# Optimization experiments

Hardware: AMD Instinct MI355X
Metric: run time of the kernel (lower is better)

The kernel has to match this reference:

```python
import jax, jax.numpy as jnp
import numpy as np

B = 4096
FEAT = 512
EMB = 64
HID = 1024
NUM_CLASSES = 64   # == option_num == noise_lib_Y.shape[0]
LIB_X = 256
LIB_Y = 256
OUT_J = 256


def setup_inputs() -> dict:
    key = jax.random.key(0)
    ks = jax.random.split(key, 16)
    s = lambda k, shape, fan: jax.random.normal(k, shape, jnp.float32) / np.sqrt(fan)
    d_in = FEAT + EMB
    return {
        "state": jax.random.normal(ks[0], (B, FEAT), jnp.float32),
        "option": jax.random.randint(ks[1], (B,), 0, NUM_CLASSES, jnp.int64),
        "embed_table": s(ks[2], (NUM_CLASSES, EMB), EMB),
        "Wx1": s(ks[3], (d_in, HID), d_in), "bx1": jnp.zeros((HID,), jnp.float32),
        "Wx2": s(ks[4], (HID, LIB_X), HID), "bx2": jnp.zeros((LIB_X,), jnp.float32),
        "Wy1": s(ks[5], (d_in, HID), d_in), "by1": jnp.zeros((HID,), jnp.float32),
        "Wy2": s(ks[6], (HID, LIB_Y), HID), "by2": jnp.zeros((LIB_Y,), jnp.float32),
        "noise_lib_X": s(ks[7], (LIB_X, OUT_J), LIB_X),
        "noise_lib_Y": s(ks[8], (NUM_CLASSES, LIB_Y, OUT_J), LIB_Y),
    }


def _mlp(x, W1, b1, W2, b2):
    # MLP_RELU, layer_num=2: Linear -> ReLU -> Linear
    h = jax.nn.relu(x @ W1 + b1)
    return h @ W2 + b2


def reference(state, option, embed_table, Wx1, bx1, Wx2, bx2,
              Wy1, by1, Wy2, by2, noise_lib_X, noise_lib_Y):
    option_embed = embed_table[option]                      # [B, EMB]
    all_state = jnp.concatenate([state, option_embed], axis=-1)
    cls_X = _mlp(all_state, Wx1, bx1, Wx2, bx2)             # [B, LIB_X]
    cls_Y = _mlp(all_state, Wy1, by1, Wy2, by2)             # [B, LIB_Y]
    # Original: einsum('bi,mij->bmj') then mask with one_hot(option).
    # Mathematically identical gather-then-matmul (honors the routing sparsity):
    noise_Y_sel = noise_lib_Y[option]                       # [B, LIB_Y, OUT_J]
    generate_noise_Y = jnp.einsum('bi,bij->bj', cls_Y, noise_Y_sel)
    generate_noise_X = cls_X @ noise_lib_X                  # [B, OUT_J]
    return (generate_noise_X, generate_noise_Y)
```

## Files before the change

kernel.cpp:

```cpp
#include <hip/hip_runtime.h>

typedef unsigned short u16;
typedef unsigned int u32;

using f32x4  = __attribute__((ext_vector_type(4))) float;
using bf16x8 = __attribute__((ext_vector_type(8))) __bf16;

#define DEV __device__ __forceinline__

DEV u16 f2bf(float f) {
  union { float f; u32 u; } x; x.f = f;
  return (u16)((x.u + 0x7fffu + ((x.u >> 16) & 1u)) >> 16);
}
DEV float bf2f(u16 h) {
  union { u32 u; float f; } x; x.u = ((u32)h) << 16;
  return x.f;
}

DEV void async_cp16(const u16* g, u16* l) {
  __builtin_amdgcn_global_load_lds((const __attribute__((address_space(1))) void*)g,
                                   (__attribute__((address_space(3))) void*)l,
                                   16, 0, 0);
}

static constexpr int BATCH = 4096;
static constexpr int FEAT  = 512;
static constexpr int EMB   = 64;
static constexpr int HID   = 1024;
static constexpr int NC    = 64;
static constexpr int DIN   = 576;
static constexpr int LIB   = 256;

DEV void detect_lite(const u32* __restrict__ sraw, const u32* __restrict__ oraw,
                     int* isf32, int* ostr) {
  __shared__ int cib, conz;
  const int t = threadIdx.x;
  if (t == 0) { cib = 0; conz = 0; }
  u32 w = sraw[t];
  u32 e = (w >> 7) & 0xFFu;
  unsigned long long m1 = __ballot(e >= 100 && e <= 142);
  unsigned long long m2 = __ballot((t & 1) && oraw[t] != 0);
  __syncthreads();
  if ((t & 63) == 0) {
    atomicAdd(&cib, __popcll(m1));
    atomicAdd(&conz, __popcll(m2));
  }
  __syncthreads();
  *isf32 = (cib < 128) ? 1 : 0;
  *ostr  = (conz == 0) ? 2 : 1;
}

DEV void do_transpose64(const void* __restrict__ in, size_t in_off,
                        u16* __restrict__ out, int R, int C,
                        int by, int bx, int isf32) {
  __shared__ u16 tile[64 * 72];
  const int t = threadIdx.x;
  {
    const int r = t >> 2, c0 = (t & 3) * 16;
    size_t off = in_off + (size_t)(by * 64 + r) * C + (bx * 64 + c0);
    u16 v[16];
    if (isf32) {
      const float4* s = (const float4*)((const float*)in + off);
      float4 a0 = s[0], a1 = s[1], a2 = s[2], a3 = s[3];
      v[0] = f2bf(a0.x); v[1] = f2bf(a0.y); v[2]  = f2bf(a0.z); v[3]  = f2bf(a0.w);
      v[4] = f2bf(a1.x); v[5] = f2bf(a1.y); v[6]  = f2bf(a1.z); v[7]  = f2bf(a1.w);
      v[8] = f2bf(a2.x); v[9] = f2bf(a2.y); v[10] = f2bf(a2.z); v[11] = f2bf(a2.w);
      v[12] = f2bf(a3.x); v[13] = f2bf(a3.y); v[14] = f2bf(a3.z); v[15] = f2bf(a3.w);
    } else {
      const uint4* s = (const uint4*)((const u16*)in + off);
      *(uint4*)&v[0] = s[0];
      *(uint4*)&v[8] = s[1];
    }
    *(uint4*)&tile[r * 72 + c0]     = *(uint4*)&v[0];
    *(uint4*)&tile[r * 72 + c0 + 8] = *(uint4*)&v[8];
  }
  __syncthreads();
  {
    const int c = t & 63, rs = (t >> 6) * 16;
    u16 w[16];
#pragma unroll
    for (int i = 0; i < 16; ++i) w[i] = tile[(rs + i) * 72 + c];
    size_t oo = (size_t)(bx * 64 + c) * R + (by * 64 + rs);
    *(uint4*)&out[oo]     = *(uint4*)&w[0];
    *(uint4*)&out[oo + 8] = *(uint4*)&w[8];
  }
}

struct PrepArgs {
  const void *state, *emb, *Wx1, *Wy1, *Wx2, *Wy2, *nX;
  const int* opt;
  u16 *all_state, *WT1x, *WT1y, *WT2x, *WT2y, *XT;
};
static constexpr int PB_CONCAT = BATCH * 36 / 256;
static constexpr int PB_WT1 = (DIN / 64) * (HID / 64);
static constexpr int PB_WT2 = (HID / 64) * (LIB / 64);
static constexpr int PB_XT  = (LIB / 64) * (LIB / 64);
static constexpr int PREP_BLOCKS = PB_CONCAT + 2 * PB_WT1 + 2 * PB_WT2 + PB_XT;

__global__ __launch_bounds__(256) void prep_k(PrepArgs a) {
  int isf32, os;
  detect_lite((const u32*)a.state, (const u32*)a.opt, &isf32, &os);
  int bid = blockIdx.x;
  if (bid < PB_CONCAT) {
    int idx = bid * 256 + threadIdx.x;
    int b = idx / 36, ch = idx % 36;
    const void* base;
    size_t srcoff;
    if (ch < 32) { base = a.state; srcoff = (size_t)b * FEAT + ch * 16; }
    else {
      base = a.emb;
      srcoff = (size_t)a.opt[(size_t)b * os] * EMB + (ch - 32) * 16;
    }
    u16 o[16];
    if (isf32) {
      const float4* s = (const float4*)((const float*)base + srcoff);
      float4 a0 = s[0], a1 = s[1], a2 = s[2], a3 = s[3];
      o[0] = f2bf(a0.x); o[1] = f2bf(a0.y); o[2]  = f2bf(a0.z); o[3]  = f2bf(a0.w);
      o[4] = f2bf(a1.x); o[5] = f2bf(a1.y); o[6]  = f2bf(a1.z); o[7]  = f2bf(a1.w);
      o[8] = f2bf(a2.x); o[9] = f2bf(a2.y); o[10] = f2bf(a2.z); o[11] = f2bf(a2.w);
      o[12] = f2bf(a3.x); o[13] = f2bf(a3.y); o[14] = f2bf(a3.z); o[15] = f2bf(a3.w);
    } else {
      const uint4* s = (const uint4*)((const u16*)base + srcoff);
      *(uint4*)&o[0] = s[0];
      *(uint4*)&o[8] = s[1];
    }
    u16* dst = a.all_state + (size_t)b * DIN + ch * 16;
    *(uint4*)dst       = *(const uint4*)&o[0];
    *(uint4*)(dst + 8) = *(const uint4*)&o[8];
    return;
  }
  bid -= PB_CONCAT;
  if (bid < PB_WT1) { do_transpose64(a.Wx1, 0, a.WT1x, DIN, HID, bid >> 4, bid & 15, isf32); return; }
  bid -= PB_WT1;
  if (bid < PB_WT1) { do_transpose64(a.Wy1, 0, a.WT1y, DIN, HID, bid >> 4, bid & 15, isf32); return; }
  bid -= PB_WT1;
  if (bid < PB_WT2) { do_transpose64(a.Wx2, 0, a.WT2x, HID, LIB, bid >> 2, bid & 3, isf32); return; }
  bid -= PB_WT2;
  if (bid < PB_WT2) { do_transpose64(a.Wy2, 0, a.WT2y, HID, LIB, bid >> 2, bid & 3, isf32); return; }
  bid -= PB_WT2;
  do_transpose64(a.nX, 0, a.XT, LIB, LIB, bid >> 2, bid & 3, isf32);
}

template <int BM, int BN, bool RELU>
DEV void gemm_tile(u16* lds, const u16* __restrict__ A, const u16* __restrict__ Bt,
                   const void* bias, void* C, int N, int K, int m0, int n0,
                   int isf32, bool cf32) {
  constexpr int WM = BM / 2, WN = BN / 2, TM = WM / 16, TN = WN / 16;
  u16* As = lds;
  u16* Bs = lds + BM * 64;
  const int t = threadIdx.x;
  const int lane = t & 63, wid = t >> 6;
  const int wm = wid >> 1, wn = wid & 1;
  const int lr = lane & 15, lq = lane >> 4;
  f32x4 acc[TM][TN] = {};
  for (int k0 = 0; k0 < K; k0 += 64) {
    __syncthreads();
#pragma unroll
    for (int sl = 0; sl < 2; ++sl) {
#pragma unroll
      for (int u = 0; u < BM / 64; ++u) {
        int unit = u * 256 + t;
        int r = unit >> 2, c8 = (unit & 3) * 8;
        async_cp16(A + (size_t)(m0 + r) * K + (k0 + sl * 32 + c8),
                   &As[(sl * BM + r) * 32 + c8]);
      }
#pragma unroll
      for (int u = 0; u < BN / 64; ++u) {
        int unit = u * 256 + t;
        int r = unit >> 2, c8 = (unit & 3) * 8;
        async_cp16(Bt + (size_t)(n0 + r) * K + (k0 + sl * 32 + c8),
                   &Bs[(sl * BN + r) * 32 + c8]);
      }
    }
    __syncthreads();
#pragma unroll
    for (int sl = 0; sl < 2; ++sl) {
      bf16x8 av[TM], bv[TN];
#pragma unroll
      for (int i = 0; i < TM; ++i)
        av[i] = *(const bf16x8*)&As[(sl * BM + wm * WM + i * 16 + lr) * 32 + lq * 8];
#pragma unroll
      for (int j = 0; j < TN; ++j)
        bv[j] = *(const bf16x8*)&Bs[(sl * BN + wn * WN + j * 16 + lr) * 32 + lq * 8];
#pragma unroll
      for (int i = 0; i < TM; ++i)
#pragma unroll
        for (int j = 0; j < TN; ++j)
          acc[i][j] = __builtin_amdgcn_mfma_f32_16x16x32_bf16(av[i], bv[j], acc[i][j], 0, 0, 0);
    }
  }
#pragma unroll
  for (int j = 0; j < TN; ++j) {
    const int gc = n0 + wn * WN + j * 16 + lr;
    const float bval = bias
        ? (isf32 ? ((const float*)bias)[gc] : bf2f(((const u16*)bias)[gc]))
        : 0.f;
#pragma unroll
    for (int i = 0; i < TM; ++i) {
      const int gr = m0 + wm * WM + i * 16 + lq * 4;
#pragma unroll
      for (int r = 0; r < 4; ++r) {
        float v = acc[i][j][r] + bval;
        if (RELU) v = fmaxf(v, 0.f);
        const size_t idx = (size_t)(gr + r) * N + gc;
        if (cf32) ((float*)C)[idx] = v;
        else      ((u16*)C)[idx] = f2bf(v);
      }
    }
  }
}

struct GArg { const u16* A; const u16* Bt; const void* bias; void* C; int cflag; };

template <int BM, int BN, bool RELU>
__global__ __launch_bounds__(256) void gemm_bt(GArg g0, GArg g1, int N, int K,
                                               const void* state, const void* opt) {
  __shared__ __align__(16) u16 lds[(BM + BN) * 64];
  int isf32, os;
  detect_lite((const u32*)state, (const u32*)opt, &isf32, &os);
  const GArg g = blockIdx.z ? g1 : g0;
  gemm_tile<BM, BN, RELU>(lds, g.A, g.Bt, g.bias, g.C, N, K,
                          blockIdx.y * BM, blockIdx.x * BN,
                          isf32, g.cflag && isf32);
}

struct TailArgs {
  const u16 *cls_x, *XT, *cls_y;
  const void *nY, *state;
  const int* opt;
  void* out;
};

__global__ __launch_bounds__(256) void tail_k(TailArgs a) {
  __shared__ __align__(16) u16 lds[25216];
  __shared__ int wcnt[4], lbase;
  int isf32, os;
  detect_lite((const u32*)a.state, (const u32*)a.opt, &isf32, &os);
  const bool of32 = (isf32 != 0);
  const int t = threadIdx.x;
  const int lane = t & 63, w = t >> 6, lr = lane & 15, lq = lane >> 4;

  if (blockIdx.x < 256) {
    const int m0 = (blockIdx.x >> 2) * 64, n0 = (blockIdx.x & 3) * 64;
    gemm_tile<64, 64, false>(lds, a.cls_x, a.XT, nullptr, a.out,
                             LIB, LIB, m0, n0, isf32, of32);
    return;
  }

  u16* Bts  = lds;
  u16* Asm  = lds + 16896;
  u16* list = lds + 21120;
  const int rb = blockIdx.x - 256;
  const int m = rb >> 2, n0 = (rb & 3) * 64;

#pragma unroll
  for (int pass = 0; pass < 4; ++pass) {
    const int k = pass * 64 + (t >> 2), nc = (t & 3) * 16;
    const size_t off = ((size_t)m * LIB + k) * LIB + n0 + nc;
    u16 v[16];
    if (isf32) {
      const float4* s = (const float4*)((const float*)a.nY + off);
      float4 a0 = s[0], a1 = s[1], a2 = s[2], a3 = s[3];
      v[0] = f2bf(a0.x); v[1] = f2bf(a0.y); v[2]  = f2bf(a0.z); v[3]  = f2bf(a0.w);
      v[4] = f2bf(a1.x); v[5] = f2bf(a1.y); v[6]  = f2bf(a1.z); v[7]  = f2bf(a1.w);
      v[8] = f2bf(a2.x); v[9] = f2bf(a2.y); v[10] = f2bf(a2.z); v[11] = f2bf(a2.w);
      v[12] = f2bf(a3.x); v[13] = f2bf(a3.y); v[14] = f2bf(a3.z); v[15] = f2bf(a3.w);
    } else {
      const uint4* s = (const uint4*)((const u16*)a.nY + off);
      *(uint4*)&v[0] = s[0];
      *(uint4*)&v[8] = s[1];
    }
#pragma unroll
    for (int j = 0; j < 16; ++j) Bts[(nc + j) * 264 + k] = v[j];
  }

  if (t == 0) lbase = 0;
  __syncthreads();
  for (int base = 0; base < BATCH; base += 256) {
    const int b = base + t;
    const int e = a.opt[(size_t)b * os];
    unsigned long long mk = __ballot(e == m);
    if (lane == 0) wcnt[w] = __popcll(mk);
    __syncthreads();
    int wpre = lbase;
    for (int i = 0; i < w; ++i) wpre += wcnt[i];
    const int mypre = __popcll(mk & ((1ull << lane) - 1ull));
    if (e == m) list[wpre + mypre] = (u16)b;
    __syncthreads();
    if (t == 0) lbase += wcnt[0] + wcnt[1] + wcnt[2] + wcnt[3];
  }
  __syncthreads();
  const int cnt = lbase;
  const size_t out_off = (size_t)BATCH * LIB;

  for (int ch = 0; ch < cnt; ch += 16) {
    __syncthreads();
    {
      const int r = t >> 4, cb = (t & 15) * 16;
      if (ch + r < cnt) {
        const u16* src = a.cls_y + (size_t)list[ch + r] * LIB + cb;
        *(uint4*)&Asm[r * 264 + cb]     = *(const uint4*)src;
        *(uint4*)&Asm[r * 264 + cb + 8] = *(const uint4*)(src + 8);
      } else {
        uint4 z{0, 0, 0, 0};
        *(uint4*)&Asm[r * 264 + cb]     = z;
        *(uint4*)&Asm[r * 264 + cb + 8] = z;
      }
    }
    __syncthreads();
    f32x4 acc = {};
#pragma unroll
    for (int kk = 0; kk < LIB; kk += 32) {
      bf16x8 av = *(const bf16x8*)&Asm[lr * 264 + kk + lq * 8];
      bf16x8 bv = *(const bf16x8*)&Bts[(w * 16 + lr) * 264 + kk + lq * 8];
      acc = __builtin_amdgcn_mfma_f32_16x16x32_bf16(av, bv, acc, 0, 0, 0);
    }
#pragma unroll
    for (int r = 0; r < 4; ++r) {
      const int rowc = lq * 4 + r;
      if (ch + rowc < cnt) {
        const size_t oi = out_off + (size_t)list[ch + rowc] * LIB
                        + (n0 + w * 16 + lr);
        if (of32) ((float*)a.out)[oi] = acc[r];
        else      ((u16*)a.out)[oi] = f2bf(acc[r]);
      }
    }
  }
}

extern "C" void kernel_launch(void* const* d_in, const int* in_sizes, int n_in,
                              void* d_out, int out_size, void* d_ws, size_t ws_size,
                              hipStream_t stream) {
  char* p = (char*)d_ws;
  auto alloc = [&](size_t bytes) { char* r = p; p += (bytes + 255) & ~(size_t)255; return r; };
  u16* all_state = (u16*)alloc((size_t)BATCH * DIN * 2);
  u16* h_x   = (u16*)alloc((size_t)BATCH * HID * 2);
  u16* h_y   = (u16*)alloc((size_t)BATCH * HID * 2);
  u16* cls_x = (u16*)alloc((size_t)BATCH * LIB * 2);
  u16* cls_y = (u16*)alloc((size_t)BATCH * LIB * 2);
  u16* WT1x  = (u16*)alloc((size_t)HID * DIN * 2);
  u16* WT1y  = (u16*)alloc((size_t)HID * DIN * 2);
  u16* WT2x  = (u16*)alloc((size_t)LIB * HID * 2);
  u16* WT2y  = (u16*)alloc((size_t)LIB * HID * 2);
  u16* XT    = (u16*)alloc((size_t)LIB * LIB * 2);

  const void* state = d_in[0];
  const void* opt   = d_in[1];

  PrepArgs pa;
  pa.state = state; pa.opt = (const int*)opt; pa.emb = d_in[2];
  pa.Wx1 = d_in[3]; pa.Wx2 = d_in[5]; pa.Wy1 = d_in[7]; pa.Wy2 = d_in[9];
  pa.nX = d_in[11];
  pa.all_state = all_state; pa.WT1x = WT1x; pa.WT1y = WT1y;
  pa.WT2x = WT2x; pa.WT2y = WT2y; pa.XT = XT;
  prep_k<<<PREP_BLOCKS, 256, 0, stream>>>(pa);

  GArg g1x{all_state, WT1x, d_in[4], h_x, 0}, g1y{all_state, WT1y, d_in[8], h_y, 0};
  gemm_bt<128, 128, true><<<dim3(HID / 128, BATCH / 128, 2), 256, 0, stream>>>(
      g1x, g1y, HID, DIN, state, opt);

  GArg g2x{h_x, WT2x, d_in[6], cls_x, 0}, g2y{h_y, WT2y, d_in[10], cls_y, 0};
  gemm_bt<64, 64, false><<<dim3(LIB / 64, BATCH / 64, 2), 256, 0, stream>>>(
      g2x, g2y, LIB, HID, state, opt);

  TailArgs ta{cls_x, XT, cls_y, d_in[12], state, (const int*)opt, d_out};
  tail_k<<<512, 256, 0, stream>>>(ta);
}
```

Baseline: 156.6 us.

## Fold noise_lib_X into second X-layer weights to skip the cls_X GEMM

The product Wx2 @ noise_lib_X and the bias bx2 @ noise_lib_X are precomputed in the prep kernel, so the second X-branch GEMM writes generate_noise_X directly and the tail kernel no longer runs the cls_X @ XT GEMM. This removes one B×256×256 GEMM and the cls_x round trip through memory, in exchange for a small weight-only GEMM and a serial bias dot product in prep, plus an extra bf16 rounding of the fused weight. The GEMM grid axes are also swapped so that blockIdx.x walks the batch rows.

```diff
diff --git a/kernel.cpp b/kernel.cpp
--- a/kernel.cpp
+++ b/kernel.cpp
@@ -50,27 +50,30 @@
   *ostr  = (conz == 0) ? 2 : 1;
 }
 
-DEV void do_transpose64(const void* __restrict__ in, size_t in_off,
+DEV void load16_bf(u16* v, const void* __restrict__ in, size_t off, int isf32) {
+  if (isf32) {
+    const float4* s = (const float4*)((const float*)in + off);
+    float4 a0 = s[0], a1 = s[1], a2 = s[2], a3 = s[3];
+    v[0] = f2bf(a0.x); v[1] = f2bf(a0.y); v[2]  = f2bf(a0.z); v[3]  = f2bf(a0.w);
+    v[4] = f2bf(a1.x); v[5] = f2bf(a1.y); v[6]  = f2bf(a1.z); v[7]  = f2bf(a1.w);
+    v[8] = f2bf(a2.x); v[9] = f2bf(a2.y); v[10] = f2bf(a2.z); v[11] = f2bf(a2.w);
+    v[12] = f2bf(a3.x); v[13] = f2bf(a3.y); v[14] = f2bf(a3.z); v[15] = f2bf(a3.w);
+  } else {
+    const uint4* s = (const uint4*)((const u16*)in + off);
+    *(uint4*)&v[0] = s[0];
+    *(uint4*)&v[8] = s[1];
+  }
+}
+
+DEV void do_transpose64(u16* lds, const void* __restrict__ in,
                         u16* __restrict__ out, int R, int C,
                         int by, int bx, int isf32) {
-  __shared__ u16 tile[64 * 72];
+  u16* tile = lds;
   const int t = threadIdx.x;
   {
     const int r = t >> 2, c0 = (t & 3) * 16;
-    size_t off = in_off + (size_t)(by * 64 + r) * C + (bx * 64 + c0);
     u16 v[16];
-    if (isf32) {
-      const float4* s = (const float4*)((const float*)in + off);
-      float4 a0 = s[0], a1 = s[1], a2 = s[2], a3 = s[3];
-      v[0] = f2bf(a0.x); v[1] = f2bf(a0.y); v[2]  = f2bf(a0.z); v[3]  = f2bf(a0.w);
-      v[4] = f2bf(a1.x); v[5] = f2bf(a1.y); v[6]  = f2bf(a1.z); v[7]  = f2bf(a1.w);
-      v[8] = f2bf(a2.x); v[9] = f2bf(a2.y); v[10] = f2bf(a2.z); v[11] = f2bf(a2.w);
-      v[12] = f2bf(a3.x); v[13] = f2bf(a3.y); v[14] = f2bf(a3.z); v[15] = f2bf(a3.w);
-    } else {
-      const uint4* s = (const uint4*)((const u16*)in + off);
-      *(uint4*)&v[0] = s[0];
-      *(uint4*)&v[8] = s[1];
-    }
+    load16_bf(v, in, (size_t)(by * 64 + r) * C + (bx * 64 + c0), isf32);
     *(uint4*)&tile[r * 72 + c0]     = *(uint4*)&v[0];
     *(uint4*)&tile[r * 72 + c0 + 8] = *(uint4*)&v[8];
   }
@@ -86,18 +89,80 @@
   }
 }
 
+DEV void tgemm_task(u16* lds, const void* __restrict__ nX,
+                    const void* __restrict__ Wx2, u16* __restrict__ T,
+                    int mt, int nt, int isf32) {
+  u16* Als = lds;
+  u16* Bls = lds + 64 * 264;
+  const int t = threadIdx.x;
+  const int m0 = mt * 64, q0 = nt * 64;
+#pragma unroll
+  for (int pass = 0; pass < 4; ++pass) {
+    const int i = pass * 64 + (t >> 2), jc = (t & 3) * 16;
+    u16 v[16];
+    load16_bf(v, nX, (size_t)i * LIB + m0 + jc, isf32);
+#pragma unroll
+    for (int j = 0; j < 16; ++j) Als[(jc + j) * 264 + i] = v[j];
+  }
+  const int lane = t & 63, wid = t >> 6;
+  const int wm = wid >> 1, wn = wid & 1;
+  const int lr = lane & 15, lq = lane >> 4;
+  f32x4 acc[2][2] = {};
+  for (int k0 = 0; k0 < LIB; k0 += 64) {
+    __syncthreads();
+    {
+      const int q = t >> 2, ic = (t & 3) * 16;
+      u16 w16[16];
+      load16_bf(w16, Wx2, (size_t)(q0 + q) * LIB + k0 + ic, isf32);
+      const int sl = ic >> 5;
+      u16* dst = &Bls[(sl * 64 + q) * 32 + (ic & 31)];
+      *(uint4*)dst       = *(uint4*)&w16[0];
+      *(uint4*)(dst + 8) = *(uint4*)&w16[8];
+    }
+    __syncthreads();
+#pragma unroll
+    for (int sl = 0; sl < 2; ++sl) {
+      bf16x8 av[2], bv[2];
+#pragma unroll
+      for (int i2 = 0; i2 < 2; ++i2)
+        av[i2] = *(const bf16x8*)&Als[(wm * 32 + i2 * 16 + lr) * 264 + k0 + sl * 32 + lq * 8];
+#pragma unroll
+      for (int j2 = 0; j2 < 2; ++j2)
+        bv[j2] = *(const bf16x8*)&Bls[(sl * 64 + wn * 32 + j2 * 16 + lr) * 32 + lq * 8];
+#pragma unroll
+      for (int i2 = 0; i2 < 2; ++i2)
+#pragma unroll
+        for (int j2 = 0; j2 < 2; ++j2)
+          acc[i2][j2] = __builtin_amdgcn_mfma_f32_16x16x32_bf16(av[i2], bv[j2], acc[i2][j2], 0, 0, 0);
+    }
+  }
+#pragma unroll
+  for (int j2 = 0; j2 < 2; ++j2) {
+    const int gc = q0 + wn * 32 + j2 * 16 + lr;
+#pragma unroll
+    for (int i2 = 0; i2 < 2; ++i2) {
+      const int gr = m0 + wm * 32 + i2 * 16 + lq * 4;
+#pragma unroll
+      for (int r = 0; r < 4; ++r)
+        T[(size_t)(gr + r) * HID + gc] = f2bf(acc[i2][j2][r]);
+    }
+  }
+}
+
 struct PrepArgs {
-  const void *state, *emb, *Wx1, *Wy1, *Wx2, *Wy2, *nX;
+  const void *state, *emb, *Wx1, *Wy1, *Wy2, *Wx2, *nX, *bx2;
   const int* opt;
-  u16 *all_state, *WT1x, *WT1y, *WT2x, *WT2y, *XT;
+  u16 *all_state, *WT1x, *WT1y, *WT2y, *T;
+  float* b2x;
 };
 static constexpr int PB_CONCAT = BATCH * 36 / 256;
 static constexpr int PB_WT1 = (DIN / 64) * (HID / 64);
 static constexpr int PB_WT2 = (HID / 64) * (LIB / 64);
-static constexpr int PB_XT  = (LIB / 64) * (LIB / 64);
-static constexpr int PREP_BLOCKS = PB_CONCAT + 2 * PB_WT1 + 2 * PB_WT2 + PB_XT;
+static constexpr int PB_TG  = (LIB / 64) * (HID / 64);
+static constexpr int PREP_BLOCKS = PB_CONCAT + 2 * PB_WT1 + PB_WT2 + PB_TG + 1;
 
 __global__ __launch_bounds__(256) void prep_k(PrepArgs a) {
+  __shared__ __align__(16) u16 plds[64 * 264 + 128 * 32];
   int isf32, os;
   detect_lite((const u32*)a.state, (const u32*)a.opt, &isf32, &os);
   int bid = blockIdx.x;
@@ -112,39 +177,37 @@
       srcoff = (size_t)a.opt[(size_t)b * os] * EMB + (ch - 32) * 16;
     }
     u16 o[16];
-    if (isf32) {
-      const float4* s = (const float4*)((const float*)base + srcoff);
-      float4 a0 = s[0], a1 = s[1], a2 = s[2], a3 = s[3];
-      o[0] = f2bf(a0.x); o[1] = f2bf(a0.y); o[2]  = f2bf(a0.z); o[3]  = f2bf(a0.w);
-      o[4] = f2bf(a1.x); o[5] = f2bf(a1.y); o[6]  = f2bf(a1.z); o[7]  = f2bf(a1.w);
-      o[8] = f2bf(a2.x); o[9] = f2bf(a2.y); o[10] = f2bf(a2.z); o[11] = f2bf(a2.w);
-      o[12] = f2bf(a3.x); o[13] = f2bf(a3.y); o[14] = f2bf(a3.z); o[15] = f2bf(a3.w);
-    } else {
-      const uint4* s = (const uint4*)((const u16*)base + srcoff);
-      *(uint4*)&o[0] = s[0];
-      *(uint4*)&o[8] = s[1];
-    }
+    load16_bf(o, base, srcoff, isf32);
     u16* dst = a.all_state + (size_t)b * DIN + ch * 16;
     *(uint4*)dst       = *(const uint4*)&o[0];
     *(uint4*)(dst + 8) = *(const uint4*)&o[8];
     return;
   }
   bid -= PB_CONCAT;
-  if (bid < PB_WT1) { do_transpose64(a.Wx1, 0, a.WT1x, DIN, HID, bid >> 4, bid & 15, isf32); return; }
+  if (bid < PB_WT1) { do_transpose64(plds, a.Wx1, a.WT1x, DIN, HID, bid >> 4, bid & 15, isf32); return; }
   bid -= PB_WT1;
-  if (bid < PB_WT1) { do_transpose64(a.Wy1, 0, a.WT1y, DIN, HID, bid >> 4, bid & 15, isf32); return; }
+  if (bid < PB_WT1) { do_transpose64(plds, a.Wy1, a.WT1y, DIN, HID, bid >> 4, bid & 15, isf32); return; }
   bid -= PB_WT1;
-  if (bid < PB_WT2) { do_transpose64(a.Wx2, 0, a.WT2x, HID, LIB, bid >> 2, bid & 3, isf32); return; }
+  if (bid < PB_WT2) { do_transpose64(plds, a.Wy2, a.WT2y, HID, LIB, bid >> 2, bid & 3, isf32); return; }
   bid -= PB_WT2;
-  if (bid < PB_WT2) { do_transpose64(a.Wy2, 0, a.WT2y, HID, LIB, bid >> 2, bid & 3, isf32); return; }
-  bid -= PB_WT2;
-  do_transpose64(a.nX, 0, a.XT, LIB, LIB, bid >> 2, bid & 3, isf32);
+  if (bid < PB_TG) { tgemm_task(plds, a.nX, a.Wx2, a.T, bid & 3, bid >> 2, isf32); return; }
+  {
+    const int j = threadIdx.x;
+    float acc = 0.f;
+    for (int i = 0; i < LIB; ++i) {
+      float s = isf32 ? ((const float*)a.bx2)[i] : bf2f(((const u16*)a.bx2)[i]);
+      float v = isf32 ? ((const float*)a.nX)[(size_t)i * LIB + j]
+                      : bf2f(((const u16*)a.nX)[(size_t)i * LIB + j]);
+      acc += s * v;
+    }
+    a.b2x[j] = acc;
+  }
 }
 
 template <int BM, int BN, bool RELU>
 DEV void gemm_tile(u16* lds, const u16* __restrict__ A, const u16* __restrict__ Bt,
                    const void* bias, void* C, int N, int K, int m0, int n0,
-                   int isf32, bool cf32) {
+                   int isf32, bool cf32, bool bf32) {
   constexpr int WM = BM / 2, WN = BN / 2, TM = WM / 16, TN = WN / 16;
   u16* As = lds;
   u16* Bs = lds + BM * 64;
@@ -193,7 +256,7 @@
   for (int j = 0; j < TN; ++j) {
     const int gc = n0 + wn * WN + j * 16 + lr;
     const float bval = bias
-        ? (isf32 ? ((const float*)bias)[gc] : bf2f(((const u16*)bias)[gc]))
+        ? (bf32 ? ((const float*)bias)[gc] : bf2f(((const u16*)bias)[gc]))
         : 0.f;
 #pragma unroll
     for (int i = 0; i < TM; ++i) {
@@ -210,7 +273,7 @@
   }
 }
 
-struct GArg { const u16* A; const u16* Bt; const void* bias; void* C; int cflag; };
+struct GArg { const u16* A; const u16* Bt; const void* bias; void* C; int cflag; int bflag; };
 
 template <int BM, int BN, bool RELU>
 __global__ __launch_bounds__(256) void gemm_bt(GArg g0, GArg g1, int N, int K,
@@ -220,12 +283,12 @@
   detect_lite((const u32*)state, (const u32*)opt, &isf32, &os);
   const GArg g = blockIdx.z ? g1 : g0;
   gemm_tile<BM, BN, RELU>(lds, g.A, g.Bt, g.bias, g.C, N, K,
-                          blockIdx.y * BM, blockIdx.x * BN,
-                          isf32, g.cflag && isf32);
+                          blockIdx.x * BM, blockIdx.y * BN,
+                          isf32, g.cflag && isf32, g.bflag || isf32);
 }
 
 struct TailArgs {
-  const u16 *cls_x, *XT, *cls_y;
+  const u16* cls_y;
   const void *nY, *state;
   const int* opt;
   void* out;
@@ -240,36 +303,16 @@
   const int t = threadIdx.x;
   const int lane = t & 63, w = t >> 6, lr = lane & 15, lq = lane >> 4;
 
-  if (blockIdx.x < 256) {
-    const int m0 = (blockIdx.x >> 2) * 64, n0 = (blockIdx.x & 3) * 64;
-    gemm_tile<64, 64, false>(lds, a.cls_x, a.XT, nullptr, a.out,
-                             LIB, LIB, m0, n0, isf32, of32);
-    return;
-  }
-
   u16* Bts  = lds;
   u16* Asm  = lds + 16896;
   u16* list = lds + 21120;
-  const int rb = blockIdx.x - 256;
-  const int m = rb >> 2, n0 = (rb & 3) * 64;
+  const int m = blockIdx.x & 63, n0 = (blockIdx.x >> 6) * 64;
 
 #pragma unroll
   for (int pass = 0; pass < 4; ++pass) {
     const int k = pass * 64 + (t >> 2), nc = (t & 3) * 16;
-    const size_t off = ((size_t)m * LIB + k) * LIB + n0 + nc;
     u16 v[16];
-    if (isf32) {
-      const float4* s = (const float4*)((const float*)a.nY + off);
-      float4 a0 = s[0], a1 = s[1], a2 = s[2], a3 = s[3];
-      v[0] = f2bf(a0.x); v[1] = f2bf(a0.y); v[2]  = f2bf(a0.z); v[3]  = f2bf(a0.w);
-      v[4] = f2bf(a1.x); v[5] = f2bf(a1.y); v[6]  = f2bf(a1.z); v[7]  = f2bf(a1.w);
-      v[8] = f2bf(a2.x); v[9] = f2bf(a2.y); v[10] = f2bf(a2.z); v[11] = f2bf(a2.w);
-      v[12] = f2bf(a3.x); v[13] = f2bf(a3.y); v[14] = f2bf(a3.z); v[15] = f2bf(a3.w);
-    } else {
-      const uint4* s = (const uint4*)((const u16*)a.nY + off);
-      *(uint4*)&v[0] = s[0];
-      *(uint4*)&v[8] = s[1];
-    }
+    load16_bf(v, a.nY, ((size_t)m * LIB + k) * LIB + n0 + nc, isf32);
 #pragma unroll
     for (int j = 0; j < 16; ++j) Bts[(nc + j) * 264 + k] = v[j];
   }
@@ -336,33 +379,34 @@
   u16* all_state = (u16*)alloc((size_t)BATCH * DIN * 2);
   u16* h_x   = (u16*)alloc((size_t)BATCH * HID * 2);
   u16* h_y   = (u16*)alloc((size_t)BATCH * HID * 2);
-  u16* cls_x = (u16*)alloc((size_t)BATCH * LIB * 2);
   u16* cls_y = (u16*)alloc((size_t)BATCH * LIB * 2);
   u16* WT1x  = (u16*)alloc((size_t)HID * DIN * 2);
   u16* WT1y  = (u16*)alloc((size_t)HID * DIN * 2);
-  u16* WT2x  = (u16*)alloc((size_t)LIB * HID * 2);
   u16* WT2y  = (u16*)alloc((size_t)LIB * HID * 2);
-  u16* XT    = (u16*)alloc((size_t)LIB * LIB * 2);
+  u16* T     = (u16*)alloc((size_t)LIB * HID * 2);
+  float* b2x = (float*)alloc((size_t)LIB * 4);
 
   const void* state = d_in[0];
   const void* opt   = d_in[1];
 
   PrepArgs pa;
   pa.state = state; pa.opt = (const int*)opt; pa.emb = d_in[2];
-  pa.Wx1 = d_in[3]; pa.Wx2 = d_in[5]; pa.Wy1 = d_in[7]; pa.Wy2 = d_in[9];
-  pa.nX = d_in[11];
-  pa.all_state = all_state; pa.WT1x = WT1x; pa.WT1y = WT1y;
-  pa.WT2x = WT2x; pa.WT2y = WT2y; pa.XT = XT;
+  pa.Wx1 = d_in[3]; pa.Wx2 = d_in[5]; pa.bx2 = d_in[6];
+  pa.Wy1 = d_in[7]; pa.Wy2 = d_in[9]; pa.nX = d_in[11];
+  pa.all_state = all_state; pa.WT1x = WT1x; pa.WT1y = WT1y; pa.WT2y = WT2y;
+  pa.T = T; pa.b2x = b2x;
   prep_k<<<PREP_BLOCKS, 256, 0, stream>>>(pa);
 
-  GArg g1x{all_state, WT1x, d_in[4], h_x, 0}, g1y{all_state, WT1y, d_in[8], h_y, 0};
-  gemm_bt<128, 128, true><<<dim3(HID / 128, BATCH / 128, 2), 256, 0, stream>>>(
+  GArg g1x{all_state, WT1x, d_in[4], h_x, 0, 0};
+  GArg g1y{all_state, WT1y, d_in[8], h_y, 0, 0};
+  gemm_bt<128, 128, true><<<dim3(BATCH / 128, HID / 128, 2), 256, 0, stream>>>(
       g1x, g1y, HID, DIN, state, opt);
 
-  GArg g2x{h_x, WT2x, d_in[6], cls_x, 0}, g2y{h_y, WT2y, d_in[10], cls_y, 0};
-  gemm_bt<64, 64, false><<<dim3(LIB / 64, BATCH / 64, 2), 256, 0, stream>>>(
+  GArg g2x{h_x, T, b2x, d_out, 1, 1};
+  GArg g2y{h_y, WT2y, d_in[10], cls_y, 0, 0};
+  gemm_bt<64, 64, false><<<dim3(BATCH / 64, LIB / 64, 2), 256, 0, stream>>>(
       g2x, g2y, LIB, HID, state, opt);
 
-  TailArgs ta{cls_x, XT, cls_y, d_in[12], state, (const int*)opt, d_out};
-  tail_k<<<512, 256, 0, stream>>>(ta);
-}
+  TailArgs ta{cls_y, d_in[12], state, (const int*)opt, d_out};
+  tail_k<<<256, 256, 0, stream>>>(ta);
+}
```

New measurement: 186.3 us. +18.9%, slower.
